# Kernel optimization log

Hardware: AMD Instinct MI355X
Metric: run time of the kernel (lower is better)

## Reference

```python
import jax, jax.numpy as jnp
from jax import lax
import numpy as np

NUM_STATES = 12            # 3 + num_hidden_states(9)
PERC_CH = 4 * NUM_STATES   # 48
HID = 96                   # num_hidden_features
N, H, W = 8, 512, 512


def setup_inputs() -> dict:
    key = jax.random.key(0)
    ks = jax.random.split(key, 7)
    x = jax.random.normal(ks[0], (N, NUM_STATES, H, W), dtype=jnp.float32)
    mask = jax.random.randint(ks[1], (N, NUM_STATES, H, W), 0, 2, dtype=jnp.int32)
    # perception 3x3 conv params (Conv2d default has bias)
    fan_p = NUM_STATES * 9
    pw = jax.random.uniform(ks[2], (PERC_CH, NUM_STATES, 3, 3), jnp.float32,
                            -1.0 / np.sqrt(fan_p), 1.0 / np.sqrt(fan_p))
    pb = jax.random.uniform(ks[3], (PERC_CH,), jnp.float32,
                            -1.0 / np.sqrt(fan_p), 1.0 / np.sqrt(fan_p))
    # update rule: 1x1 conv (PERC_CH->HID, bias) -> ReLU -> 1x1 conv (HID->NUM_STATES, no bias)
    w1 = jax.random.uniform(ks[4], (HID, PERC_CH), jnp.float32,
                            -1.0 / np.sqrt(PERC_CH), 1.0 / np.sqrt(PERC_CH))
    b1 = jax.random.uniform(ks[5], (HID,), jnp.float32,
                            -1.0 / np.sqrt(PERC_CH), 1.0 / np.sqrt(PERC_CH))
    w2 = jax.random.uniform(ks[6], (NUM_STATES, HID), jnp.float32,
                            -1.0 / np.sqrt(HID), 1.0 / np.sqrt(HID))
    return {"x": x, "pw": pw, "pb": pb, "w1": w1, "b1": b1, "w2": w2, "mask": mask}


def reference(x, pw, pb, w1, b1, w2, mask):
    # circular pad (matches F.pad mode='circular' with (1,1,1,1))
    y = jnp.pad(x, ((0, 0), (0, 0), (1, 1), (1, 1)), mode='wrap')
    # 3x3 VALID conv on padded input -> [N, 48, H, W]
    perc = lax.conv_general_dilated(
        y, pw, window_strides=(1, 1), padding='VALID',
        dimension_numbers=('NCHW', 'OIHW', 'NCHW')) + pb[None, :, None, None]
    # 1x1 conv -> ReLU -> 1x1 conv (per-pixel MLP)
    h = jax.nn.relu(jnp.einsum('nchw,fc->nfhw', perc, w1) + b1[None, :, None, None])
    update = jnp.einsum('nfhw,of->nohw', h, w2)
    # stochastic mask + residual
    update = update * mask.astype(x.dtype)
    return x + update
```

## Files before the change

### kernel.cpp

```cpp
#include <hip/hip_runtime.h>

typedef __attribute__((ext_vector_type(8))) short s16x8;
typedef __attribute__((ext_vector_type(4))) float f32x4;
typedef __attribute__((ext_vector_type(4))) int i32x4;

#define HW2 262144
#define NSTATE 12

__device__ __forceinline__ unsigned f2b_bits(float f) {
  unsigned u = __builtin_bit_cast(unsigned, f);
  return (u + 0x7fffu + ((u >> 16) & 1u)) >> 16;
}

__global__ void ca_prep(const float* __restrict__ pw, const float* __restrict__ pb,
                        const float* __restrict__ w1, const float* __restrict__ b1,
                        const float* __restrict__ w2,
                        short* __restrict__ A1, short* __restrict__ A2,
                        float* __restrict__ cb) {
  const int b = blockIdx.x, t = threadIdx.x;
  if (b < 30) {
    const int kf = b / 6, mf = b % 6;
    const int blk = t >> 4;
    const int row = 16 * mf + (t & 15);
    short v[8];
#pragma unroll
    for (int e = 0; e < 8; ++e) {
      const int k = 32 * kf + 8 * blk + e;
      const int sh = k >> 4, s = k & 15;
      float acc = 0.f;
      if (sh < 9 && s < 12) {
        const int ky = sh / 3, kx = sh % 3;
        for (int c = 0; c < 48; ++c)
          acc += w1[row * 48 + c] * pw[((c * 12 + s) * 3 + ky) * 3 + kx];
      }
      v[e] = (short)f2b_bits(acc);
    }
    short* dst = A1 + (b * 64 + t) * 8;
#pragma unroll
    for (int e = 0; e < 8; ++e) dst[e] = v[e];
  } else {
    const int blk = t >> 4, row = t & 15;
    for (int f = 0; f < 3; ++f) {
      short* dst = A2 + (f * 64 + t) * 8;
#pragma unroll
      for (int e = 0; e < 8; ++e) {
        const int k = 16 * (2 * f + (e >> 2)) + 4 * blk + (e & 3);
        const float val = (row < 12) ? w2[row * 96 + k] : 0.f;
        dst[e] = (short)f2b_bits(val);
      }
    }
    for (int j = t; j < 96; j += 64) {
      float a = b1[j];
      for (int c = 0; c < 48; ++c) a += w1[j * 48 + c] * pb[c];
      cb[j] = a;
    }
  }
}

#define TY 8
#define TX 64
#define LYS 10
#define LXS 66

#define EP_ADDR(gid) ((base_n + col) * HW2 + ((y0 + ((gid) >> 2)) << 9) + x0 + (((gid) & 3) << 4) + 4 * blk)

__launch_bounds__(256, 2)
__global__ void ca_main(const float* __restrict__ x, const int* __restrict__ mask,
                        const short* wsA1,
                        const short* __restrict__ wsA2,
                        const float* __restrict__ wscb, float* out ) {
  __shared__ short lds[LYS * LXS * 16 + 8];
  const int ZOFF = LYS * LXS * 16;

  const int tid = threadIdx.x;
  const int b = blockIdx.x;
  const int n = b >> 9;
  const int rem = b & 511;
  const int y0 = (rem >> 3) * TY;
  const int x0 = (rem & 7) * TX;

  const int lane = tid & 63;
  const int blk = lane >> 4;
  const int col = lane & 15;

  s16x8 A1[5][6];
#pragma unroll
  for (int kf = 0; kf < 5; ++kf)
#pragma unroll
    for (int mf = 0; mf < 6; ++mf)
      A1[kf][mf] = *(const s16x8*)(wsA1 + ((kf * 6 + mf) * 64 + lane) * 8);
  s16x8 A2[3];
#pragma unroll
  for (int f = 0; f < 3; ++f) A2[f] = *(const s16x8*)(wsA2 + (f * 64 + lane) * 8);
  f32x4 cbv[6];
#pragma unroll
  for (int mf = 0; mf < 6; ++mf)
    cbv[mf] = *(const f32x4*)(wscb + 16 * mf + 4 * blk);

  if (tid == 0) { *(i32x4*)(lds + ZOFF) = (i32x4){0, 0, 0, 0}; }

  const int base_n = n * NSTATE;
  for (int p = tid; p < LYS * LXS; p += 256) {
    const int ly = p / LXS;
    const int lx = p - ly * LXS;
    const int gy = (y0 - 1 + ly) & 511;
    const int gx = (x0 - 1 + lx) & 511;
    const int gbase = base_n * HW2 + (gy << 9) + gx;
    unsigned bs[12];
#pragma unroll
    for (int s = 0; s < 12; ++s) bs[s] = f2b_bits(x[gbase + s * HW2]);
    i32x4 v0 = {(int)(bs[0] | (bs[1] << 16)), (int)(bs[2] | (bs[3] << 16)),
                (int)(bs[4] | (bs[5] << 16)), (int)(bs[6] | (bs[7] << 16))};
    i32x4 v1 = {(int)(bs[8] | (bs[9] << 16)), (int)(bs[10] | (bs[11] << 16)), 0, 0};
    *(i32x4*)(lds + p * 16) = v0;
    *(i32x4*)(lds + p * 16 + 8) = v1;
  }
  __syncthreads();

  const int wave = tid >> 6;

  f32x4 cxq = {0.f, 0.f, 0.f, 0.f};
  i32x4 cmq = {0, 0, 0, 0};
  if (col < 12) {
    const int a = EP_ADDR(wave * 8);
    cxq = *(const f32x4*)(x + a);
    cmq = *(const i32x4*)(mask + a);
  }

#pragma unroll 1
  for (int i = 0; i < 8; ++i) {
    const int gid = wave * 8 + i;
    const int ty = gid >> 2;
    const int tx0 = (gid & 3) << 4;

    s16x8 b1f[5];
#pragma unroll
    for (int kf = 0; kf < 5; ++kf) {
      const int sh = 2 * kf + (blk >> 1);
      const short* ap;
      if (sh < 9) {
        const int ky = sh / 3, kx = sh - 3 * (sh / 3);
        ap = lds + ((ty + ky) * LXS + (tx0 + col + kx)) * 16 + 8 * (blk & 1);
      } else {
        ap = lds + ZOFF;
      }
      b1f[kf] = *(const s16x8*)ap;
    }

    f32x4 nxq = {0.f, 0.f, 0.f, 0.f};
    i32x4 nmq = {0, 0, 0, 0};
    if (col < 12) {
      const int a = EP_ADDR(wave * 8 + ((i + 1) & 7));
      nxq = *(const f32x4*)(x + a);
      nmq = *(const i32x4*)(mask + a);
    }

    f32x4 hacc[6];
#pragma unroll
    for (int mf = 0; mf < 6; ++mf) hacc[mf] = cbv[mf];
#pragma unroll
    for (int kf = 0; kf < 5; ++kf)
#pragma unroll
      for (int mf = 0; mf < 6; ++mf)
        hacc[mf] = __builtin_amdgcn_mfma_f32_16x16x32_bf16(A1[kf][mf], b1f[kf], hacc[mf], 0, 0, 0);

    f32x4 upd = {0.f, 0.f, 0.f, 0.f};
#pragma unroll
    for (int f = 0; f < 3; ++f) {
      s16x8 b2f;
#pragma unroll
      for (int e = 0; e < 8; ++e) {
        float v = hacc[2 * f + (e >> 2)][e & 3];
        v = v > 0.f ? v : 0.f;
        b2f[e] = (short)f2b_bits(v);
      }
      upd = __builtin_amdgcn_mfma_f32_16x16x32_bf16(b2f, A2[f], upd, 0, 0, 0);
    }

    if (col < 12) {
      const int a = EP_ADDR(gid);
      f32x4 o;
#pragma unroll
      for (int r = 0; r < 4; ++r) o[r] = cxq[r] + upd[r] * (float)cmq[r];
      *(f32x4*)(out + a) = o;
    }
    cxq = nxq;
    cmq = nmq;
  }
}

extern "C" void kernel_launch(void* const* d_in, const int* in_sizes, int n_in,
                              void* d_out, int out_size, void* d_ws, size_t ws_size,
                              hipStream_t stream) {
  const float* x  = (const float*)d_in[0];
  const float* pw = (const float*)d_in[1];
  const float* pb = (const float*)d_in[2];
  const float* w1 = (const float*)d_in[3];
  const float* b1 = (const float*)d_in[4];
  const float* w2 = (const float*)d_in[5];
  const int* mask = (const int*)d_in[6];
  float* out = (float*)d_out;

  short* A1 = (short*)d_ws;
  short* A2 = (short*)((char*)d_ws + 30720);
  float* cb = (float*)((char*)d_ws + 30720 + 3072);

  ca_prep<<<31, 64, 0, stream>>>(pw, pb, w1, b1, w2, A1, A2, cb);
  ca_main<<<4096, 256, 0, stream>>>(x, mask, A1, A2, cb, out);
}
```

Baseline: 321.8 us.

## Process two tiles per block with double-buffered LDS and vectorized halo loads

Each block now handles two 8x64 tiles. The second tile's input is loaded into registers while the first tile is computed, then written to a second LDS buffer. The halo staging changes from scalar per-pixel gathers of 12 channels to float4 row loads plus separate edge-column loads, and bf16 packing now uses the hardware v_cvt_pk_bf16_f32 instruction. Bias values move from registers to LDS. The cost is higher register pressure from the prefetch registers, doubled LDS use, and scalar 2-byte scattered LDS writes that may cause bank conflicts.

```diff
diff --git a/kernel.cpp b/kernel.cpp
--- a/kernel.cpp
+++ b/kernel.cpp
@@ -3,6 +3,7 @@
 typedef __attribute__((ext_vector_type(8))) short s16x8;
 typedef __attribute__((ext_vector_type(4))) float f32x4;
 typedef __attribute__((ext_vector_type(4))) int i32x4;
+typedef __attribute__((ext_vector_type(2))) int i32x2;
 
 #define HW2 262144
 #define NSTATE 12
@@ -10,6 +11,12 @@
 __device__ __forceinline__ unsigned f2b_bits(float f) {
   unsigned u = __builtin_bit_cast(unsigned, f);
   return (u + 0x7fffu + ((u >> 16) & 1u)) >> 16;
+}
+
+__device__ __forceinline__ unsigned cvt_pk_bf16(float lo, float hi) {
+  unsigned r;
+  asm("v_cvt_pk_bf16_f32 %0, %1, %2" : "=v"(r) : "v"(lo), "v"(hi));
+  return r;
 }
 
 __global__ void ca_prep(const float* __restrict__ pw, const float* __restrict__ pb,
@@ -57,31 +64,29 @@
   }
 }
 
-#define TY 8
-#define TX 64
-#define LYS 10
-#define LXS 66
-
-#define EP_ADDR(gid) ((base_n + col) * HW2 + ((y0 + ((gid) >> 2)) << 9) + x0 + (((gid) & 3) << 4) + 4 * blk)
+#define BUFS 10560
 
 __launch_bounds__(256, 2)
 __global__ void ca_main(const float* __restrict__ x, const int* __restrict__ mask,
                         const short* wsA1,
                         const short* __restrict__ wsA2,
                         const float* __restrict__ wscb, float* out ) {
-  __shared__ short lds[LYS * LXS * 16 + 8];
-  const int ZOFF = LYS * LXS * 16;
+  __shared__ short lds[2 * BUFS + 8 + 192];
+  const int ZOFF = 2 * BUFS;
+  float* cbl = (float*)(lds + ZOFF + 8);
 
   const int tid = threadIdx.x;
-  const int b = blockIdx.x;
-  const int n = b >> 9;
-  const int rem = b & 511;
-  const int y0 = (rem >> 3) * TY;
-  const int x0 = (rem & 7) * TX;
-
   const int lane = tid & 63;
   const int blk = lane >> 4;
   const int col = lane & 15;
+  const int wave = tid >> 6;
+
+  const int gt0 = blockIdx.x * 2;
+  const int n = gt0 >> 9;
+  const int base_n = n * NSTATE;
+  const int rem0 = gt0 & 511, rem1 = rem0 + 1;
+  const int y00 = (rem0 >> 3) * 8, x00 = (rem0 & 7) * 64;
+  const int y01 = (rem1 >> 3) * 8, x01 = (rem1 & 7) * 64;
 
   s16x8 A1[5][6];
 #pragma unroll
@@ -92,101 +97,148 @@
   s16x8 A2[3];
 #pragma unroll
   for (int f = 0; f < 3; ++f) A2[f] = *(const s16x8*)(wsA2 + (f * 64 + lane) * 8);
-  f32x4 cbv[6];
-#pragma unroll
-  for (int mf = 0; mf < 6; ++mf)
-    cbv[mf] = *(const f32x4*)(wscb + 16 * mf + 4 * blk);
-
-  if (tid == 0) { *(i32x4*)(lds + ZOFF) = (i32x4){0, 0, 0, 0}; }
-
-  const int base_n = n * NSTATE;
-  for (int p = tid; p < LYS * LXS; p += 256) {
-    const int ly = p / LXS;
-    const int lx = p - ly * LXS;
-    const int gy = (y0 - 1 + ly) & 511;
-    const int gx = (x0 - 1 + lx) & 511;
-    const int gbase = base_n * HW2 + (gy << 9) + gx;
-    unsigned bs[12];
-#pragma unroll
-    for (int s = 0; s < 12; ++s) bs[s] = f2b_bits(x[gbase + s * HW2]);
-    i32x4 v0 = {(int)(bs[0] | (bs[1] << 16)), (int)(bs[2] | (bs[3] << 16)),
-                (int)(bs[4] | (bs[5] << 16)), (int)(bs[6] | (bs[7] << 16))};
-    i32x4 v1 = {(int)(bs[8] | (bs[9] << 16)), (int)(bs[10] | (bs[11] << 16)), 0, 0};
-    *(i32x4*)(lds + p * 16) = v0;
-    *(i32x4*)(lds + p * 16 + 8) = v1;
-  }
+
+  f32x4 rx[8];
+  float hx = 0.f;
+
+  auto stage_load = [&](int y0, int x0) {
+#pragma unroll
+    for (int i = 0; i < 8; ++i) {
+      const int task = tid + (i << 8);
+      if (task < 1920) {
+        const int rq = task / 12;
+        const int s = task - rq * 12;
+        const int q = rq & 15, ly = rq >> 4;
+        const int gy = (y0 - 1 + ly) & 511;
+        rx[i] = *(const f32x4*)(x + ((base_n + s) << 18) + (gy << 9) + x0 + (q << 2));
+      }
+    }
+    if (tid < 240) {
+      const int r = tid >> 1, side = tid & 1;
+      const int ly = r / 12;
+      const int s = r - ly * 12;
+      const int gy = (y0 - 1 + ly) & 511;
+      const int gx = side ? ((x0 + 64) & 511) : ((x0 - 1) & 511);
+      hx = x[((base_n + s) << 18) + (gy << 9) + gx];
+    }
+  };
+
+  auto stage_write = [&](short* buf) {
+#pragma unroll
+    for (int i = 0; i < 8; ++i) {
+      const int task = tid + (i << 8);
+      if (task < 1920) {
+        const int rq = task / 12;
+        const int s = task - rq * 12;
+        const int q = rq & 15, ly = rq >> 4;
+        const int pix = ly * 66 + 1 + (q << 2);
+        const unsigned w0 = cvt_pk_bf16(rx[i][0], rx[i][1]);
+        const unsigned w1v = cvt_pk_bf16(rx[i][2], rx[i][3]);
+        buf[(pix + 0) * 16 + s] = (short)w0;
+        buf[(pix + 1) * 16 + s] = (short)(w0 >> 16);
+        buf[(pix + 2) * 16 + s] = (short)w1v;
+        buf[(pix + 3) * 16 + s] = (short)(w1v >> 16);
+      }
+    }
+    if (tid < 240) {
+      const int r = tid >> 1, side = tid & 1;
+      const int ly = r / 12;
+      const int s = r - ly * 12;
+      buf[(ly * 66 + side * 65) * 16 + s] = (short)f2b_bits(hx);
+    }
+  };
+
+  auto compute_tile = [&](const short* buf, int y0, int x0) {
+    f32x4 cxq = {0.f, 0.f, 0.f, 0.f};
+    i32x4 cmq = {0, 0, 0, 0};
+    auto ep_addr = [&](int gid) {
+      return (base_n + col) * HW2 + ((y0 + (gid >> 2)) << 9) + x0 + ((gid & 3) << 4) + 4 * blk;
+    };
+    if (col < 12) {
+      const int a = ep_addr(wave * 8);
+      cxq = *(const f32x4*)(x + a);
+      cmq = *(const i32x4*)(mask + a);
+    }
+#pragma unroll 1
+    for (int i = 0; i < 8; ++i) {
+      const int gid = wave * 8 + i;
+      const int ty = gid >> 2;
+      const int tx0 = (gid & 3) << 4;
+
+      s16x8 b1f[5];
+#pragma unroll
+      for (int kf = 0; kf < 5; ++kf) {
+        const int sh = 2 * kf + (blk >> 1);
+        const short* ap;
+        if (sh < 9) {
+          const int ky = sh / 3, kx = sh - 3 * (sh / 3);
+          ap = buf + ((ty + ky) * 66 + (tx0 + col + kx)) * 16 + 8 * (blk & 1);
+        } else {
+          ap = lds + ZOFF;
+        }
+        b1f[kf] = *(const s16x8*)ap;
+      }
+
+      f32x4 nxq = {0.f, 0.f, 0.f, 0.f};
+      i32x4 nmq = {0, 0, 0, 0};
+      if (col < 12) {
+        const int a = ep_addr(wave * 8 + ((i + 1) & 7));
+        nxq = *(const f32x4*)(x + a);
+        nmq = *(const i32x4*)(mask + a);
+      }
+
+      f32x4 hacc[6];
+#pragma unroll
+      for (int mf = 0; mf < 6; ++mf) hacc[mf] = *(const f32x4*)(cbl + 16 * mf + 4 * blk);
+#pragma unroll
+      for (int kf = 0; kf < 5; ++kf)
+#pragma unroll
+        for (int mf = 0; mf < 6; ++mf)
+          hacc[mf] = __builtin_amdgcn_mfma_f32_16x16x32_bf16(A1[kf][mf], b1f[kf], hacc[mf], 0, 0, 0);
+
+      f32x4 upd = {0.f, 0.f, 0.f, 0.f};
+#pragma unroll
+      for (int f = 0; f < 3; ++f) {
+        unsigned w[4];
+#pragma unroll
+        for (int j = 0; j < 4; ++j) {
+          const float a = fmaxf(hacc[2 * f + (j >> 1)][2 * (j & 1)], 0.f);
+          const float bb = fmaxf(hacc[2 * f + (j >> 1)][2 * (j & 1) + 1], 0.f);
+          w[j] = cvt_pk_bf16(a, bb);
+        }
+        const i32x4 wv = {(int)w[0], (int)w[1], (int)w[2], (int)w[3]};
+        const s16x8 b2f = __builtin_bit_cast(s16x8, wv);
+        upd = __builtin_amdgcn_mfma_f32_16x16x32_bf16(b2f, A2[f], upd, 0, 0, 0);
+      }
+
+      if (col < 12) {
+        const int a = ep_addr(gid);
+        f32x4 o;
+#pragma unroll
+        for (int r = 0; r < 4; ++r) o[r] = cxq[r] + upd[r] * (float)cmq[r];
+        *(f32x4*)(out + a) = o;
+      }
+      cxq = nxq;
+      cmq = nmq;
+    }
+  };
+
+  stage_load(y00, x00);
+
+  for (int i = tid; i < 2 * 660; i += 256)
+    *(i32x2*)(lds + i * 16 + 12) = (i32x2){0, 0};
+  if (tid == 0) *(i32x4*)(lds + ZOFF) = (i32x4){0, 0, 0, 0};
+  if (tid < 24) *(f32x4*)(cbl + tid * 4) = *(const f32x4*)(wscb + tid * 4);
+
+  stage_write(lds);
   __syncthreads();
 
-  const int wave = tid >> 6;
-
-  f32x4 cxq = {0.f, 0.f, 0.f, 0.f};
-  i32x4 cmq = {0, 0, 0, 0};
-  if (col < 12) {
-    const int a = EP_ADDR(wave * 8);
-    cxq = *(const f32x4*)(x + a);
-    cmq = *(const i32x4*)(mask + a);
-  }
-
-#pragma unroll 1
-  for (int i = 0; i < 8; ++i) {
-    const int gid = wave * 8 + i;
-    const int ty = gid >> 2;
-    const int tx0 = (gid & 3) << 4;
-
-    s16x8 b1f[5];
-#pragma unroll
-    for (int kf = 0; kf < 5; ++kf) {
-      const int sh = 2 * kf + (blk >> 1);
-      const short* ap;
-      if (sh < 9) {
-        const int ky = sh / 3, kx = sh - 3 * (sh / 3);
-        ap = lds + ((ty + ky) * LXS + (tx0 + col + kx)) * 16 + 8 * (blk & 1);
-      } else {
-        ap = lds + ZOFF;
-      }
-      b1f[kf] = *(const s16x8*)ap;
-    }
-
-    f32x4 nxq = {0.f, 0.f, 0.f, 0.f};
-    i32x4 nmq = {0, 0, 0, 0};
-    if (col < 12) {
-      const int a = EP_ADDR(wave * 8 + ((i + 1) & 7));
-      nxq = *(const f32x4*)(x + a);
-      nmq = *(const i32x4*)(mask + a);
-    }
-
-    f32x4 hacc[6];
-#pragma unroll
-    for (int mf = 0; mf < 6; ++mf) hacc[mf] = cbv[mf];
-#pragma unroll
-    for (int kf = 0; kf < 5; ++kf)
-#pragma unroll
-      for (int mf = 0; mf < 6; ++mf)
-        hacc[mf] = __builtin_amdgcn_mfma_f32_16x16x32_bf16(A1[kf][mf], b1f[kf], hacc[mf], 0, 0, 0);
-
-    f32x4 upd = {0.f, 0.f, 0.f, 0.f};
-#pragma unroll
-    for (int f = 0; f < 3; ++f) {
-      s16x8 b2f;
-#pragma unroll
-      for (int e = 0; e < 8; ++e) {
-        float v = hacc[2 * f + (e >> 2)][e & 3];
-        v = v > 0.f ? v : 0.f;
-        b2f[e] = (short)f2b_bits(v);
-      }
-      upd = __builtin_amdgcn_mfma_f32_16x16x32_bf16(b2f, A2[f], upd, 0, 0, 0);
-    }
-
-    if (col < 12) {
-      const int a = EP_ADDR(gid);
-      f32x4 o;
-#pragma unroll
-      for (int r = 0; r < 4; ++r) o[r] = cxq[r] + upd[r] * (float)cmq[r];
-      *(f32x4*)(out + a) = o;
-    }
-    cxq = nxq;
-    cmq = nmq;
-  }
+  stage_load(y01, x01);
+  compute_tile(lds, y00, x00);
+  stage_write(lds + BUFS);
+  __syncthreads();
+
+  compute_tile(lds + BUFS, y01, x01);
 }
 
 extern "C" void kernel_launch(void* const* d_in, const int* in_sizes, int n_in,
@@ -206,5 +258,5 @@
   float* cb = (float*)((char*)d_ws + 30720 + 3072);
 
   ca_prep<<<31, 64, 0, stream>>>(pw, pb, w1, b1, w2, A1, A2, cb);
-  ca_main<<<4096, 256, 0, stream>>>(x, mask, A1, A2, cb, out);
-}
+  ca_main<<<2048, 256, 0, stream>>>(x, mask, A1, A2, cb, out);
+}
```

Result: slower. 346.5 us (+7.7%).

## Stage mask as bytes in LDS, use hardware bf16 pack, move bias to LDS

Applied to the files above, without the earlier changes.

The int32 mask tile is now loaded up front with coalesced 16-byte loads, packed to one byte per pixel, and staged in LDS. Previously the epilogue loaded it per iteration through a strided, 12-of-16-lane pattern. The ReLU-to-bf16 conversion now uses the packed v_cvt_pk_bf16_f32 instruction instead of manual rounding arithmetic. The bias vector moves from registers into LDS, which frees VGPRs at the cost of extra LDS reads each iteration. Shared memory use grows, and the mask fetch adds time to the prologue before the barrier.

```diff
diff --git a/kernel.cpp b/kernel.cpp
--- a/kernel.cpp
+++ b/kernel.cpp
@@ -10,6 +10,12 @@
 __device__ __forceinline__ unsigned f2b_bits(float f) {
   unsigned u = __builtin_bit_cast(unsigned, f);
   return (u + 0x7fffu + ((u >> 16) & 1u)) >> 16;
+}
+
+__device__ __forceinline__ unsigned cvt_pk_bf16(float lo, float hi) {
+  unsigned r;
+  asm("v_cvt_pk_bf16_f32 %0, %1, %2" : "=v"(r) : "v"(lo), "v"(hi));
+  return r;
 }
 
 __global__ void ca_prep(const float* __restrict__ pw, const float* __restrict__ pb,
@@ -57,10 +63,9 @@
   }
 }
 
-#define TY 8
-#define TX 64
-#define LYS 10
-#define LXS 66
+#define ZOFF 10560
+#define CBOFF 10568
+#define MOFF 10760
 
 #define EP_ADDR(gid) ((base_n + col) * HW2 + ((y0 + ((gid) >> 2)) << 9) + x0 + (((gid) & 3) << 4) + 4 * blk)
 
@@ -69,19 +74,22 @@
                         const short* wsA1,
                         const short* __restrict__ wsA2,
                         const float* __restrict__ wscb, float* out ) {
-  __shared__ short lds[LYS * LXS * 16 + 8];
-  const int ZOFF = LYS * LXS * 16;
+  __shared__ short lds[13880];
+  float* cbl = (float*)(lds + CBOFF);
+  char* mlds = (char*)(lds + MOFF);
 
   const int tid = threadIdx.x;
   const int b = blockIdx.x;
   const int n = b >> 9;
   const int rem = b & 511;
-  const int y0 = (rem >> 3) * TY;
-  const int x0 = (rem & 7) * TX;
+  const int y0 = (rem >> 3) * 8;
+  const int x0 = (rem & 7) * 64;
 
   const int lane = tid & 63;
   const int blk = lane >> 4;
   const int col = lane & 15;
+  const int wave = tid >> 6;
+  const int base_n = n * NSTATE;
 
   s16x8 A1[5][6];
 #pragma unroll
@@ -92,17 +100,26 @@
   s16x8 A2[3];
 #pragma unroll
   for (int f = 0; f < 3; ++f) A2[f] = *(const s16x8*)(wsA2 + (f * 64 + lane) * 8);
-  f32x4 cbv[6];
-#pragma unroll
-  for (int mf = 0; mf < 6; ++mf)
-    cbv[mf] = *(const f32x4*)(wscb + 16 * mf + 4 * blk);
 
   if (tid == 0) { *(i32x4*)(lds + ZOFF) = (i32x4){0, 0, 0, 0}; }
-
-  const int base_n = n * NSTATE;
-  for (int p = tid; p < LYS * LXS; p += 256) {
-    const int ly = p / LXS;
-    const int lx = p - ly * LXS;
+  if (tid < 24) *(f32x4*)(cbl + tid * 4) = *(const f32x4*)(wscb + tid * 4);
+
+#pragma unroll
+  for (int i = 0; i < 6; ++i) {
+    const int task = tid + (i << 8);
+    const int s = task >> 7;
+    const int quad = task & 127;
+    const int pix = quad << 2;
+    const int ly = pix >> 6, lx = pix & 63;
+    const i32x4 mv = *(const i32x4*)(mask + ((base_n + s) << 18) + ((y0 + ly) << 9) + x0 + lx);
+    const unsigned w = (unsigned)mv[0] | ((unsigned)mv[1] << 8) |
+                       ((unsigned)mv[2] << 16) | ((unsigned)mv[3] << 24);
+    *(unsigned*)(mlds + s * 520 + pix) = w;
+  }
+
+  for (int p = tid; p < 660; p += 256) {
+    const int ly = p / 66;
+    const int lx = p - ly * 66;
     const int gy = (y0 - 1 + ly) & 511;
     const int gx = (x0 - 1 + lx) & 511;
     const int gbase = base_n * HW2 + (gy << 9) + gx;
@@ -117,15 +134,8 @@
   }
   __syncthreads();
 
-  const int wave = tid >> 6;
-
   f32x4 cxq = {0.f, 0.f, 0.f, 0.f};
-  i32x4 cmq = {0, 0, 0, 0};
-  if (col < 12) {
-    const int a = EP_ADDR(wave * 8);
-    cxq = *(const f32x4*)(x + a);
-    cmq = *(const i32x4*)(mask + a);
-  }
+  if (col < 12) cxq = *(const f32x4*)(x + EP_ADDR(wave * 8));
 
 #pragma unroll 1
   for (int i = 0; i < 8; ++i) {
@@ -140,24 +150,23 @@
       const short* ap;
       if (sh < 9) {
         const int ky = sh / 3, kx = sh - 3 * (sh / 3);
-        ap = lds + ((ty + ky) * LXS + (tx0 + col + kx)) * 16 + 8 * (blk & 1);
+        ap = lds + ((ty + ky) * 66 + (tx0 + col + kx)) * 16 + 8 * (blk & 1);
       } else {
         ap = lds + ZOFF;
       }
       b1f[kf] = *(const s16x8*)ap;
     }
 
+    unsigned mword = 0;
+    if (col < 12)
+      mword = *(const unsigned*)(mlds + col * 520 + (ty << 6) + tx0 + (blk << 2));
+
     f32x4 nxq = {0.f, 0.f, 0.f, 0.f};
-    i32x4 nmq = {0, 0, 0, 0};
-    if (col < 12) {
-      const int a = EP_ADDR(wave * 8 + ((i + 1) & 7));
-      nxq = *(const f32x4*)(x + a);
-      nmq = *(const i32x4*)(mask + a);
-    }
+    if (col < 12) nxq = *(const f32x4*)(x + EP_ADDR(wave * 8 + ((i + 1) & 7)));
 
     f32x4 hacc[6];
 #pragma unroll
-    for (int mf = 0; mf < 6; ++mf) hacc[mf] = cbv[mf];
+    for (int mf = 0; mf < 6; ++mf) hacc[mf] = *(const f32x4*)(cbl + 16 * mf + 4 * blk);
 #pragma unroll
     for (int kf = 0; kf < 5; ++kf)
 #pragma unroll
@@ -167,13 +176,15 @@
     f32x4 upd = {0.f, 0.f, 0.f, 0.f};
 #pragma unroll
     for (int f = 0; f < 3; ++f) {
-      s16x8 b2f;
-#pragma unroll
-      for (int e = 0; e < 8; ++e) {
-        float v = hacc[2 * f + (e >> 2)][e & 3];
-        v = v > 0.f ? v : 0.f;
-        b2f[e] = (short)f2b_bits(v);
-      }
+      unsigned w[4];
+#pragma unroll
+      for (int j = 0; j < 4; ++j) {
+        const float a = fmaxf(hacc[2 * f + (j >> 1)][2 * (j & 1)], 0.f);
+        const float bb = fmaxf(hacc[2 * f + (j >> 1)][2 * (j & 1) + 1], 0.f);
+        w[j] = cvt_pk_bf16(a, bb);
+      }
+      const i32x4 wv = {(int)w[0], (int)w[1], (int)w[2], (int)w[3]};
+      const s16x8 b2f = __builtin_bit_cast(s16x8, wv);
       upd = __builtin_amdgcn_mfma_f32_16x16x32_bf16(b2f, A2[f], upd, 0, 0, 0);
     }
 
@@ -181,11 +192,11 @@
       const int a = EP_ADDR(gid);
       f32x4 o;
 #pragma unroll
-      for (int r = 0; r < 4; ++r) o[r] = cxq[r] + upd[r] * (float)cmq[r];
+      for (int r = 0; r < 4; ++r)
+        o[r] = cxq[r] + upd[r] * (float)((mword >> (8 * r)) & 1u);
       *(f32x4*)(out + a) = o;
     }
     cxq = nxq;
-    cmq = nmq;
   }
 }
 
```

After: 316.8 us. No clear change (-1.6%).
